# Optimization experiments

Measured on AMD Instinct MI355X. Metric: run time of the kernel, lower is better.

Reference implementation:

```python
import jax, jax.numpy as jnp
import numpy as np

DEPTH = 6; HEADS = 6; DIM = 384; HD = DIM // HEADS
WS = 14; WINDOW_BLOCKS = (0, 1, 3, 4)
IMG = 512; PATCH = 16; GRID = IMG // PATCH        # 32x32 token grid
PRE_GRID = 14                                      # 224 // 16 pretrain grid
SCALE = HD ** -0.5


def layer_norm(x, w, b, eps=1e-5):
    u = x.mean(-1, keepdims=True)
    s = ((x - u) ** 2).mean(-1, keepdims=True)
    return (x - u) / jnp.sqrt(s + eps) * w + b


def get_rel_pos(size, rel_pos):
    # q_size == k_size here; relative coords in [0, 2*size-2]
    coords = jnp.arange(size)[:, None] - jnp.arange(size)[None, :] + (size - 1)
    return rel_pos[coords]  # (size, size, HD)


def attention(x, qkv_w, qkv_b, proj_w, proj_b, rel_h, rel_w):
    B, H, W, C = x.shape
    N = H * W
    qkv = (x.reshape(B, N, C) @ qkv_w.T + qkv_b).reshape(B, N, 3, HEADS, HD)
    qkv = jnp.moveaxis(qkv, 2, 0).transpose(0, 1, 3, 2, 4)  # (3,B,h,N,d)
    q, k, v = qkv[0], qkv[1], qkv[2]
    attn = jnp.einsum('bhqd,bhkd->bhqk', q * SCALE, k)
    # decomposed relative position bias (ViTDet add_decomposed_rel_pos)
    Rh = get_rel_pos(H, rel_h)  # (H,H,d)
    Rw = get_rel_pos(W, rel_w)  # (W,W,d)
    rq = q.reshape(B, HEADS, H, W, HD)
    bias_h = jnp.einsum('bnhwc,hkc->bnhwk', rq, Rh)  # (B,h,H,W,H)
    bias_w = jnp.einsum('bnhwc,wkc->bnhwk', rq, Rw)  # (B,h,H,W,W)
    attn = (attn.reshape(B, HEADS, H, W, H, W)
            + bias_h[..., :, None] + bias_w[..., None, :]).reshape(B, HEADS, N, N)
    attn = jax.nn.softmax(attn, axis=-1)
    out = jnp.einsum('bhqk,bhkd->bhqd', attn, v)
    out = out.transpose(0, 2, 1, 3).reshape(B, H, W, C)
    return out @ proj_w.T + proj_b


def window_partition(x, ws):
    B, H, W, C = x.shape
    pad_h = (ws - H % ws) % ws
    pad_w = (ws - W % ws) % ws
    x = jnp.pad(x, ((0, 0), (0, pad_h), (0, pad_w), (0, 0)))
    Hp, Wp = H + pad_h, W + pad_w
    x = x.reshape(B, Hp // ws, ws, Wp // ws, ws, C)
    x = x.transpose(0, 1, 3, 2, 4, 5).reshape(-1, ws, ws, C)
    return x, Hp, Wp


def window_unpartition(win, ws, Hp, Wp, H, W):
    B = win.shape[0] // ((Hp // ws) * (Wp // ws))
    x = win.reshape(B, Hp // ws, Wp // ws, ws, ws, -1)
    x = x.transpose(0, 1, 3, 2, 4, 5).reshape(B, Hp, Wp, -1)
    return x[:, :H, :W]


def block(x, p, windowed):
    shortcut = x
    x = layer_norm(x, p['n1w'], p['n1b'])
    if windowed:
        H, W = x.shape[1], x.shape[2]
        x, Hp, Wp = window_partition(x, WS)
    x = attention(x, p['qw'], p['qb'], p['pw'], p['pb'], p['rh'], p['rw'])
    if windowed:
        x = window_unpartition(x, WS, Hp, Wp, H, W)
    x = shortcut + x
    h = layer_norm(x, p['n2w'], p['n2b'])
    h = jax.nn.gelu(h @ p['f1w'].T + p['f1b'], approximate=False)
    return x + h @ p['f2w'].T + p['f2b']


def vit_forward(x, patch_w, patch_b, pos_embed, norm1_w, norm1_b, qkv_w, qkv_b,
                proj_w, proj_b, norm2_w, norm2_b, fc1_w, fc1_b, fc2_w, fc2_b,
                rel_pos_h, rel_pos_w):
    y = jax.lax.conv_general_dilated(
        x, patch_w, (PATCH, PATCH), 'VALID',
        dimension_numbers=('NCHW', 'OIHW', 'NCHW'))
    y = y.transpose(0, 2, 3, 1) + patch_b  # (B, GRID, GRID, DIM)
    # abs pos embed: bicubic resize from pretrain 14x14 grid to 32x32
    pos = pos_embed.reshape(1, PRE_GRID, PRE_GRID, DIM)
    pos = jax.image.resize(pos, (1, GRID, GRID, DIM), 'bicubic')
    y = y + pos
    for i in range(DEPTH):
        windowed = i in WINDOW_BLOCKS
        L = 2 * WS - 1 if windowed else 2 * GRID - 1
        p = dict(n1w=norm1_w[i], n1b=norm1_b[i], qw=qkv_w[i], qb=qkv_b[i],
                 pw=proj_w[i], pb=proj_b[i], rh=rel_pos_h[i, :L], rw=rel_pos_w[i, :L],
                 n2w=norm2_w[i], n2b=norm2_b[i], f1w=fc1_w[i], f1b=fc1_b[i],
                 f2w=fc2_w[i], f2b=fc2_b[i])
        y = block(y, p, windowed)
    return y.transpose(0, 3, 1, 2)  # (B, DIM, GRID, GRID) 'last_feat'


def setup_inputs() -> dict:
    key = jax.random.key(0)
    ks = jax.random.split(key, 10)
    B = 4
    std = 0.02
    f32 = jnp.float32
    return {
        'x': jax.random.normal(ks[0], (B, 3, IMG, IMG), f32),
        'patch_w': jax.random.normal(ks[1], (DIM, 3, PATCH, PATCH), f32) * 0.05,
        'patch_b': jnp.zeros((DIM,), f32),
        'pos_embed': jax.random.normal(ks[2], (1, PRE_GRID * PRE_GRID, DIM), f32) * std,
        'norm1_w': jnp.ones((DEPTH, DIM), f32),
        'norm1_b': jnp.zeros((DEPTH, DIM), f32),
        'qkv_w': jax.random.normal(ks[3], (DEPTH, 3 * DIM, DIM), f32) * std,
        'qkv_b': jnp.zeros((DEPTH, 3 * DIM), f32),
        'proj_w': jax.random.normal(ks[4], (DEPTH, DIM, DIM), f32) * std,
        'proj_b': jnp.zeros((DEPTH, DIM), f32),
        'norm2_w': jnp.ones((DEPTH, DIM), f32),
        'norm2_b': jnp.zeros((DEPTH, DIM), f32),
        'fc1_w': jax.random.normal(ks[5], (DEPTH, 4 * DIM, DIM), f32) * std,
        'fc1_b': jnp.zeros((DEPTH, 4 * DIM), f32),
        'fc2_w': jax.random.normal(ks[6], (DEPTH, DIM, 4 * DIM), f32) * std,
        'fc2_b': jnp.zeros((DEPTH, DIM), f32),
        'rel_pos_h': jax.random.normal(ks[7], (DEPTH, 2 * GRID - 1, HD), f32) * std,
        'rel_pos_w': jax.random.normal(ks[8], (DEPTH, 2 * GRID - 1, HD), f32) * std,
    }


def reference(x, patch_w, patch_b, pos_embed, norm1_w, norm1_b, qkv_w, qkv_b,
              proj_w, proj_b, norm2_w, norm2_b, fc1_w, fc1_b, fc2_w, fc2_b,
              rel_pos_h, rel_pos_w):
    return vit_forward(x, patch_w, patch_b, pos_embed, norm1_w, norm1_b, qkv_w, qkv_b,
                       proj_w, proj_b, norm2_w, norm2_b, fc1_w, fc1_b, fc2_w, fc2_b,
                       rel_pos_h, rel_pos_w)
```

## Files before the change

### kernel.cpp

```cpp
#include <hip/hip_runtime.h>
#include <hip/hip_bf16.h>
#include <math.h>

#define B_SZ 4
#define DIM 384
#define HEADS 6
#define HD 64
#define NTOK 4096
#define WS 14
#define NWIN 36
#define WTOK 196

typedef unsigned short u16;
typedef __bf16 bf16_t;
typedef bf16_t bf16x8 __attribute__((ext_vector_type(8)));
typedef float f32x4 __attribute__((ext_vector_type(4)));

__device__ __forceinline__ float bf2f(unsigned u) { return __uint_as_float(u << 16); }
__device__ __forceinline__ u16 f2bf(float f) {
    unsigned u = __float_as_uint(f);
    unsigned r = (u + 0x7fffu + ((u >> 16) & 1u)) >> 16;
    return (u16)r;
}
__device__ __forceinline__ unsigned pk2bf(float a, float b) {
    __hip_bfloat162 h = __float22bfloat162_rn(make_float2(a, b));
    unsigned r; __builtin_memcpy(&r, &h, 4); return r;
}

__device__ __forceinline__ void ldsload16(const u16* g, u16* l) {
    __builtin_amdgcn_global_load_lds(
        (const __attribute__((address_space(1))) unsigned int*)g,
        (__attribute__((address_space(3))) unsigned int*)l, 16, 0, 0);
}

__device__ __forceinline__ int swz(int r) { return (r ^ (r >> 2)) & 3; }

__device__ inline float cubic_keys(float x) {
    x = fabsf(x);
    if (x <= 1.f) return ((1.5f * x - 2.5f) * x) * x + 1.f;
    if (x < 2.f)  return ((-0.5f * x + 2.5f) * x - 4.f) * x + 2.f;
    return 0.f;
}

__global__ __launch_bounds__(256) void setup_kernel(
        const float* __restrict__ p0, const float* __restrict__ p1,
        const float* __restrict__ p2, const float* __restrict__ p3,
        const float* __restrict__ p4, const float* __restrict__ p5,
        u16* __restrict__ wb, const float* __restrict__ pe,
        float* __restrict__ posr, const float* __restrict__ x,
        u16* __restrict__ col) {
    int i = (blockIdx.x * 256 + threadIdx.x) * 4;
    if (i < 10918656) {
        const float* s; int off;
        if      (i <   294912) { s = p0; off = 0; }
        else if (i <  2949120) { s = p1; off = 294912; }
        else if (i <  3833856) { s = p2; off = 2949120; }
        else if (i <  7372800) { s = p3; off = 3833856; }
        else if (i < 10911744) { s = p4; off = 7372800; }
        else                   { s = p5; off = 10911744; }
        float4 v = *(const float4*)(s + (i - off));
        u16 o[4] = { f2bf(v.x), f2bf(v.y), f2bf(v.z), f2bf(v.w) };
        *(uint2*)(wb + i) = *(const uint2*)o;
        return;
    }
    i -= 10918656;
    if (i < 393216) {
        int c = i % 384;
        int g = i / 384;
        int gy = g / 32, gx = g % 32;
        float wy[14], wx[14];
        float sy = (gy + 0.5f) * (14.f / 32.f) - 0.5f;
        float sx = (gx + 0.5f) * (14.f / 32.f) - 0.5f;
        float toty = 0.f, totx = 0.f;
        #pragma unroll
        for (int k = 0; k < 14; ++k) {
            wy[k] = cubic_keys(sy - (float)k); toty += wy[k];
            wx[k] = cubic_keys(sx - (float)k); totx += wx[k];
        }
        float4 acc = {0.f, 0.f, 0.f, 0.f};
        #pragma unroll 1
        for (int iy = 0; iy < 14; ++iy) {
            if (wy[iy] == 0.f) continue;
            float4 row = {0.f, 0.f, 0.f, 0.f};
            for (int ix = 0; ix < 14; ++ix) {
                if (wx[ix] == 0.f) continue;
                float4 pv = *(const float4*)(pe + (iy * 14 + ix) * 384 + c);
                row.x += wx[ix] * pv.x; row.y += wx[ix] * pv.y;
                row.z += wx[ix] * pv.z; row.w += wx[ix] * pv.w;
            }
            acc.x += wy[iy] * row.x; acc.y += wy[iy] * row.y;
            acc.z += wy[iy] * row.z; acc.w += wy[iy] * row.w;
        }
        float inv = 1.f / (toty * totx);
        acc.x *= inv; acc.y *= inv; acc.z *= inv; acc.w *= inv;
        *(float4*)(posr + i) = acc;
        return;
    }
    i -= 393216;
    if (i < 3145728) {
        int kk = i % 768;
        int p  = i / 768;
        int b  = p / 1024;
        int ph = (p % 1024) / 32;
        int pw = p % 32;
        int c = kk / 256;
        int r = kk % 256;
        int ii = r / 16, j = r % 16;
        float4 v = *(const float4*)(x + (size_t)b * 3 * 512 * 512 +
                                    (size_t)c * 512 * 512 +
                                    (size_t)(ph * 16 + ii) * 512 + (pw * 16 + j));
        u16 o[4] = { f2bf(v.x), f2bf(v.y), f2bf(v.z), f2bf(v.w) };
        *(uint2*)(col + i) = *(const uint2*)o;
    }
}

__global__ __launch_bounds__(256) void ln_kernel(const float* __restrict__ y,
        const float* __restrict__ lw, const float* __restrict__ lb,
        u16* __restrict__ lnout)
{
    int tok = blockIdx.x * 4 + (threadIdx.x >> 6);
    int t = threadIdx.x & 63;
    size_t base = (size_t)tok * 384;
    float v[6];
    float s = 0.f;
    #pragma unroll
    for (int i = 0; i < 6; ++i) {
        v[i] = y[base + t + 64 * i]; s += v[i];
    }
    #pragma unroll
    for (int off = 32; off > 0; off >>= 1) s += __shfl_xor(s, off);
    float mean = s * (1.f / 384.f);
    float vs = 0.f;
    #pragma unroll
    for (int i = 0; i < 6; ++i) { float d = v[i] - mean; vs += d * d; }
    #pragma unroll
    for (int off = 32; off > 0; off >>= 1) vs += __shfl_xor(vs, off);
    float inv = rsqrtf(vs * (1.f / 384.f) + 1e-5f);
    u16* orow = lnout + base;
    #pragma unroll
    for (int i = 0; i < 6; ++i) {
        int c = t + 64 * i;
        orow[c] = f2bf((v[i] - mean) * inv * lw[c] + lb[c]);
    }
}

__global__ __launch_bounds__(256) void out_transpose(const float* __restrict__ y,
        float* __restrict__ outT)
{
    __shared__ float T[64][65];
    int c0 = blockIdx.x * 64, m0 = blockIdx.y * 64;
    int t = threadIdx.x;
    int cl = t & 63, wv = t >> 6;
    #pragma unroll
    for (int r = 0; r < 16; ++r) {
        int ml = wv * 16 + r;
        T[ml][cl] = y[(size_t)(m0 + ml) * 384 + c0 + cl];
    }
    __syncthreads();
    int b = m0 >> 10, g0 = m0 & 1023;
    int gl = t & 63;
    #pragma unroll
    for (int r = 0; r < 16; ++r) {
        int ccl = wv * 16 + r;
        outT[((size_t)(b * 384 + c0 + ccl)) * 1024 + g0 + gl] = T[gl][ccl];
    }
}

__global__ __launch_bounds__(256) void mfma_gemm4(
        const u16* __restrict__ A, const u16* __restrict__ Wt,
        const float* __restrict__ bias,
        u16* __restrict__ outb,
        int M, int N, int K, int act)
{
    __shared__ u16 As[2][8192];
    __shared__ u16 Bs[2][4096];
    int t = threadIdx.x;
    int lane = t & 63, wave = t >> 6;
    int wm = (wave >> 1) * 64, wn = (wave & 1) * 32;
    int m0 = blockIdx.y * 128, n0 = blockIdx.x * 64;

    int r0 = t >> 2,        c0 = ((t & 3) ^ swz(t >> 2)) * 8;
    int r1 = 64 + (t >> 2), c1 = ((t & 3) ^ swz(64 + (t >> 2))) * 8;
    const u16* a0 = A + (size_t)(m0 + r0) * K + c0;
    const u16* a1 = A + (size_t)(m0 + r1) * K + c1;
    const u16* b0 = Wt + (size_t)(n0 + r0) * K + c0;

    auto stage = [&](int k0, int buf) {
        ldsload16(a0 + k0,      &As[buf][wave * 512]);
        ldsload16(a1 + k0,      &As[buf][2048 + wave * 512]);
        ldsload16(b0 + k0,      &Bs[buf][wave * 512]);
        ldsload16(a0 + k0 + 32, &As[buf][4096 + wave * 512]);
        ldsload16(a1 + k0 + 32, &As[buf][6144 + wave * 512]);
        ldsload16(b0 + k0 + 32, &Bs[buf][2048 + wave * 512]);
    };

    f32x4 acc[4][2] = {};
    int row_a = wm + (lane & 15);
    int row_b = wn + (lane & 15);
    int lq = lane >> 4;
    int nchunks = K / 64;

    stage(0, 0);
    __syncthreads();

    for (int ci = 0; ci < nchunks; ++ci) {
        int p = ci & 1;
        bool pref = (ci + 1 < nchunks);
        if (pref) stage((ci + 1) * 64, 1 - p);
        #pragma unroll
        for (int hf = 0; hf < 2; ++hf) {
            bf16x8 af[4], bfr[2];
            #pragma unroll
            for (int i = 0; i < 4; ++i) {
                int r = row_a + i * 16;
                af[i] = *(const bf16x8*)&As[p][hf * 4096 + r * 32 + ((lq ^ swz(r)) * 8)];
            }
            #pragma unroll
            for (int j = 0; j < 2; ++j) {
                int r = row_b + j * 16;
                bfr[j] = *(const bf16x8*)&Bs[p][hf * 2048 + r * 32 + ((lq ^ swz(r)) * 8)];
            }
            #pragma unroll
            for (int i = 0; i < 4; ++i)
                #pragma unroll
                for (int j = 0; j < 2; ++j)
                    acc[i][j] = __builtin_amdgcn_mfma_f32_16x16x32_bf16(
                        af[i], bfr[j], acc[i][j], 0, 0, 0);
        }
        if (pref) __syncthreads();
    }

    int colq = lane & 15, rowq = (lane >> 4) * 4;
    #pragma unroll
    for (int i = 0; i < 4; ++i) {
        #pragma unroll
        for (int rr = 0; rr < 4; ++rr) {
            int m = m0 + wm + i * 16 + rowq + rr;
            size_t mo = (size_t)m * N;
            #pragma unroll
            for (int j = 0; j < 2; ++j) {
                int n = n0 + wn + j * 16 + colq;
                float v = acc[i][j][rr] + bias[n];
                if (act)  v = 0.5f * v * (1.f + erff(v * 0.70710678118654752f));
                outb[mo + n] = f2bf(v);
            }
        }
    }
}

__global__ __launch_bounds__(256) void mfma_gemm32(
        const u16* __restrict__ A, const u16* __restrict__ Wt,
        const float* __restrict__ bias, const float* __restrict__ posr,
        float* __restrict__ y, int addy, int M, int N, int K)
{
    __shared__ u16 As[2][4096];
    __shared__ u16 Bs[2][2048];
    int t = threadIdx.x;
    int lane = t & 63, wave = t >> 6;
    int wm = (wave >> 1) * 32, wn = (wave & 1) * 16;
    int m0 = blockIdx.y * 64, n0 = blockIdx.x * 32;

    int r0 = t >> 2, c0 = ((t & 3) ^ swz(t >> 2)) * 8;
    const u16* a0 = A + (size_t)(m0 + r0) * K + c0;
    int tb = t & 127;
    int rb = tb >> 2, cb = ((tb & 3) ^ swz(tb >> 2)) * 8;
    const u16* b0 = Wt + (size_t)(n0 + rb) * K + cb;

    auto stage = [&](int k0, int buf) {
        ldsload16(a0 + k0,      &As[buf][wave * 512]);
        ldsload16(a0 + k0 + 32, &As[buf][2048 + wave * 512]);
        if (wave < 2) ldsload16(b0 + k0,      &Bs[buf][wave * 512]);
        else          ldsload16(b0 + k0 + 32, &Bs[buf][1024 + (wave - 2) * 512]);
    };

    f32x4 acc[2] = {};
    int row_a = wm + (lane & 15);
    int row_b = wn + (lane & 15);
    int lq = lane >> 4;
    int nchunks = K / 64;

    stage(0, 0);
    __syncthreads();

    for (int ci = 0; ci < nchunks; ++ci) {
        int p = ci & 1;
        bool pref = (ci + 1 < nchunks);
        if (pref) stage((ci + 1) * 64, 1 - p);
        #pragma unroll
        for (int hf = 0; hf < 2; ++hf) {
            bf16x8 af[2], bf0;
            #pragma unroll
            for (int i = 0; i < 2; ++i) {
                int r = row_a + i * 16;
                af[i] = *(const bf16x8*)&As[p][hf * 2048 + r * 32 + ((lq ^ swz(r)) * 8)];
            }
            {
                int r = row_b;
                bf0 = *(const bf16x8*)&Bs[p][hf * 1024 + r * 32 + ((lq ^ swz(r)) * 8)];
            }
            #pragma unroll
            for (int i = 0; i < 2; ++i)
                acc[i] = __builtin_amdgcn_mfma_f32_16x16x32_bf16(
                    af[i], bf0, acc[i], 0, 0, 0);
        }
        if (pref) __syncthreads();
    }

    int colq = lane & 15, rowq = (lane >> 4) * 4;
    #pragma unroll
    for (int i = 0; i < 2; ++i) {
        #pragma unroll
        for (int rr = 0; rr < 4; ++rr) {
            int m = m0 + wm + i * 16 + rowq + rr;
            size_t mo = (size_t)m * N;
            int n = n0 + wn + colq;
            float v = acc[i][rr] + bias[n];
            if (posr) v += posr[(size_t)(m & 1023) * 384 + n];
            if (addy) v += y[mo + n];
            y[mo + n] = v;
        }
    }
}

template<int N, int W>
__global__ __launch_bounds__(256) void attn_mfma(const u16* __restrict__ qkv,
        const u16* __restrict__ qkb, const float* __restrict__ rh,
        const float* __restrict__ rw, u16* __restrict__ outb,
        float* __restrict__ opart, float* __restrict__ lpart)
{
    constexpr int JS = (W == 32) ? 64 : 32;
    constexpr int L  = (W == 32) ? 63 : 27;
    constexpr int CTR = W - 1;
    constexpr int KSPAN = (W == 32) ? 512 : 224;
    constexpr int NKT = KSPAN / 32;
    __shared__ u16 KV[11776];
    __shared__ u16 bhl[64 * 66];
    __shared__ u16 bwl[64 * 66];
    __shared__ u16 Qt[64 * 66];
    __shared__ unsigned kofs[224];

    u16* Pb = KV + 9216;
    u16* Rt = KV;

    int t = threadIdx.x, lane = t & 63, wave = t >> 6;
    int quad = lane >> 4, l15 = lane & 15;
    int uh = blockIdx.x, qb0 = blockIdx.y * 64;
    int z = (W == 32) ? blockIdx.z : 0;
    int kstart = z * KSPAN;
    int h = uh % HEADS, u = uh / HEADS;
    size_t tbase = (size_t)u * 1024;
    int wb_ = u / 9, wr = u - wb_ * 9;
    int wy = wr / 3, wx = wr - wy * 3;

    auto tok14 = [&](int iy, int ix) -> const u16* {
        int gy = wy * WS + iy, gx = wx * WS + ix;
        if (gy < 32 && gx < 32)
            return qkv + (size_t)(wb_ * 1024 + gy * 32 + gx) * 1152;
        return qkb;
    };
    auto rowptr = [&](int lq2) -> const u16* {
        if constexpr (W == 32) {
            return qkv + (tbase + lq2) * 1152;
        } else {
            int iy = lq2 / WS, ix = lq2 - iy * WS;
            return tok14(iy, ix);
        }
    };

    {
        int q = t & 63, ch0 = (t >> 6) * 16;
        int qc = qb0 + q; if (qc >= N) qc = N - 1;
        const u16* qp = rowptr(qc) + h * 64 + ch0;
        uint4 a = *(const uint4*)qp;
        uint4 b = *(const uint4*)(qp + 8);
        u16 vals[16];
        *(uint4*)vals = a; *(uint4*)(vals + 8) = b;
        #pragma unroll
        for (int c = 0; c < 16; ++c)
            Qt[(ch0 + c) * 66 + q] = ((qb0 + q) < N) ? vals[c] : (u16)0;
    }

    if constexpr (W != 32) {
        if (t < 224) {
            int kh = t / WS;
            kofs[t] = (unsigned)kh | ((unsigned)(t - kh * WS) << 16);
        }
    }

    for (int idx = t; idx < JS * 16; idx += 256) {
        int table = (idx >= JS * 8) ? 1 : 0;
        int id2 = idx & (JS * 8 - 1);
        int j = id2 >> 3, cc0 = (id2 & 7) * 8;
        const float* tab = table ? rw : rh;
        u16 tmp[8];
        if (j < L) {
            const float* src = tab + (size_t)j * 64 + cc0;
            #pragma unroll
            for (int c = 0; c < 8; ++c) tmp[c] = f2bf(src[c]);
        } else {
            #pragma unroll
            for (int c = 0; c < 8; ++c) tmp[c] = 0;
        }
        *(uint4*)&Rt[table * JS * 72 + j * 72 + cc0] = *(uint4*)tmp;
    }
    __syncthreads();

    {
        int tb0 = (W == 32) ? 0 : (wave >> 1);
        int ntb = (W == 32) ? 2 : 1;
        int jt  = (W == 32) ? wave : (wave & 1);
        for (int tt = 0; tt < ntb; ++tt) {
            int table = tb0 + tt;
            const u16* Rtt = Rt + table * JS * 72;
            bf16x8 af0 = *(const bf16x8*)&Rtt[(jt * 16 + l15) * 72 + quad * 8];
            bf16x8 af1 = *(const bf16x8*)&Rtt[(jt * 16 + l15) * 72 + 32 + quad * 8];
            u16* dst = table ? bwl : bhl;
            #pragma unroll
            for (int qt = 0; qt < 4; ++qt) {
                bf16x8 qf0, qf1;
                u16* p0 = (u16*)&qf0; u16* p1 = (u16*)&qf1;
                #pragma unroll
                for (int zz = 0; zz < 8; ++zz) {
                    p0[zz] = Qt[(quad * 8 + zz) * 66 + qt * 16 + l15];
                    p1[zz] = Qt[(32 + quad * 8 + zz) * 66 + qt * 16 + l15];
                }
                f32x4 acc = {};
                acc = __builtin_amdgcn_mfma_f32_16x16x32_bf16(af0, qf0, acc, 0, 0, 0);
                acc = __builtin_amdgcn_mfma_f32_16x16x32_bf16(af1, qf1, acc, 0, 0, 0);
                #pragma unroll
                for (int r = 0; r < 4; ++r)
                    dst[(qt * 16 + l15) * 66 + jt * 16 + quad * 4 + r] = f2bf(acc[r]);
            }
        }
    }
    __syncthreads();

    int skey = (wave * 64 + lane) >> 3;
    int sc8  = ((wave * 64 + lane) & 7) ^ (skey & 7);
    int vkey = t & 31, vch0 = (t >> 5) * 8;
    int siy = 0, six = 0, viy = 0, vix = 0;
    if constexpr (W != 32) {
        int k0 = kstart + skey;
        siy = k0 / WS; six = k0 - siy * WS;
        int k1 = kstart + vkey;
        viy = k1 / WS; vix = k1 - viy * WS;
    }
    auto adv = [](int& iy, int& ix) { ix += 4; iy += 2; if (ix >= WS) { ix -= WS; ++iy; } };

    {
        const u16* kp = (W == 32) ? qkv + (tbase + kstart + skey) * 1152
                                  : tok14(siy, six);
        ldsload16(kp + 384 + h * 64 + sc8 * 8, KV + wave * 512);
        const u16* vp = (W == 32) ? qkv + (tbase + kstart + vkey) * 1152
                                  : tok14(viy, vix);
        uint4 vv = *(const uint4*)(vp + 768 + h * 64 + vch0);
        u16 tmp[8]; *(uint4*)tmp = vv;
        u16* vdst = KV + 4096;
        #pragma unroll
        for (int c = 0; c < 8; ++c) vdst[(vch0 + c) * 40 + vkey] = tmp[c];
        if constexpr (W != 32) { adv(siy, six); adv(viy, vix); }
    }

    bf16x8 qf[2];
    #pragma unroll
    for (int hc = 0; hc < 2; ++hc) {
        u16* qv = (u16*)&qf[hc];
        #pragma unroll
        for (int j = 0; j < 8; ++j)
            qv[j] = Qt[(hc * 32 + quad * 8 + j) * 66 + wave * 16 + l15];
    }
    int qme = wave * 16 + l15;
    bool wactive = (W == 32) ? true : ((qb0 + wave * 16) < N);
    int qq = qb0 + qme; if (qq >= N) qq = N - 1;
    int qh = qq / W, qw = qq - qh * W;
    int qh13 = qh + CTR, qw13 = qw + CTR;
    float bwreg[2][4];
    if constexpr (W == 32) {
        #pragma unroll
        for (int kc2 = 0; kc2 < 2; ++kc2)
            #pragma unroll
            for (int r = 0; r < 4; ++r) {
                int keyl = kc2 * 16 + quad * 4 + r;
                bwreg[kc2][r] = bf2f(bwl[qme * 66 + (qw - keyl + CTR)]);
            }
    }

    f32x4 of[4] = {};
    float lsum = 0.f;
    __syncthreads();

    for (int kt = 0; kt < NKT; ++kt) {
        int kb = kstart + kt * 32;
        int p = kt & 1;
        const u16* ksp = KV + p * 2048;
        const u16* vtp = KV + 4096 + p * 2560;
        bool pref = (kt + 1 < NKT);
        uint4 vpref;
        if (pref) {
            const u16* kp = (W == 32) ? qkv + (tbase + kb + 32 + skey) * 1152
                                      : tok14(siy, six);
            ldsload16(kp + 384 + h * 64 + sc8 * 8, KV + (1 - p) * 2048 + wave * 512);
            const u16* vp = (W == 32) ? qkv + (tbase + kb + 32 + vkey) * 1152
                                      : tok14(viy, vix);
            vpref = *(const uint4*)(vp + 768 + h * 64 + vch0);
            if constexpr (W != 32) { adv(siy, six); adv(viy, vix); }
        }

        if (wactive) {
            f32x4 st[2] = {};
            #pragma unroll
            for (int hc = 0; hc < 2; ++hc) {
                #pragma unroll
                for (int kc2 = 0; kc2 < 2; ++kc2) {
                    int key = kc2 * 16 + l15;
                    int c8 = hc * 4 + quad;
                    int pp = key * 8 + (c8 ^ (key & 7));
                    bf16x8 kf = *(const bf16x8*)&ksp[pp * 8];
                    st[kc2] = __builtin_amdgcn_mfma_f32_16x16x32_bf16(
                        kf, qf[hc], st[kc2], 0, 0, 0);
                }
            }
            float bh_t = 0.f;
            if constexpr (W == 32) bh_t = bf2f(bhl[qme * 66 + (qh - (kb >> 5) + CTR)]);
            #pragma unroll
            for (int kc2 = 0; kc2 < 2; ++kc2) {
                float pv4[4];
                #pragma unroll
                for (int r = 0; r < 4; ++r) {
                    int keyl = kc2 * 16 + quad * 4 + r;
                    float pv;
                    if constexpr (W == 32) {
                        float b = bh_t + bwreg[kc2][r];
                        pv = __expf(fmaf(st[kc2][r], 0.125f, b));
                    } else {
                        unsigned ko = kofs[kb + keyl];
                        float b = bf2f(bhl[qme * 66 + qh13 - (int)(ko & 0xffffu)]) +
                                  bf2f(bwl[qme * 66 + qw13 - (int)(ko >> 16)]);
                        pv = __expf(fmaf(st[kc2][r], 0.125f, b));
                        if (kb + keyl >= N) pv = 0.f;
                    }
                    lsum += pv;
                    pv4[r] = pv;
                }
                uint2 pk;
                pk.x = pk2bf(pv4[0], pv4[1]);
                pk.y = pk2bf(pv4[2], pv4[3]);
                *(uint2*)&Pb[wave * 640 + l15 * 40 + kc2 * 16 + quad * 4] = pk;
            }
            bf16x8 pf = *(const bf16x8*)&Pb[wave * 640 + l15 * 40 + quad * 8];
            #pragma unroll
            for (int ca = 0; ca < 4; ++ca) {
                bf16x8 vf = *(const bf16x8*)&vtp[(ca * 16 + l15) * 40 + quad * 8];
                of[ca] = __builtin_amdgcn_mfma_f32_16x16x32_bf16(
                    vf, pf, of[ca], 0, 0, 0);
            }
        }

        if (pref) {
            u16 tmp[8]; *(uint4*)tmp = vpref;
            u16* vdst = KV + 4096 + (1 - p) * 2560;
            #pragma unroll
            for (int c = 0; c < 8; ++c) vdst[(vch0 + c) * 40 + vkey] = tmp[c];
            __syncthreads();
        }
    }

    lsum += __shfl_xor(lsum, 16);
    lsum += __shfl_xor(lsum, 32);
    int q = qb0 + qme;
    if constexpr (W == 32) {
        size_t ridx = (size_t)z * 24576 + (size_t)uh * 1024 + q;
        float* op = opart + ridx * 64;
        #pragma unroll
        for (int ca = 0; ca < 4; ++ca)
            *(float4*)&op[ca * 16 + quad * 4] = (float4){of[ca][0], of[ca][1],
                                                         of[ca][2], of[ca][3]};
        if (quad == 0) lpart[ridx] = lsum;
    } else {
        float inv = 1.f / lsum;
        if (q < N) {
            int iy = q / WS, ix = q - iy * WS;
            int gy = wy * WS + iy, gx = wx * WS + ix;
            if (gy >= 32 || gx >= 32) return;
            u16* op = outb + (size_t)(wb_ * 1024 + gy * 32 + gx) * 384 + h * 64;
            #pragma unroll
            for (int ca = 0; ca < 4; ++ca) {
                uint2 pk;
                pk.x = pk2bf(of[ca][0] * inv, of[ca][1] * inv);
                pk.y = pk2bf(of[ca][2] * inv, of[ca][3] * inv);
                *(uint2*)&op[ca * 16 + quad * 4] = pk;
            }
        }
    }
}

__global__ __launch_bounds__(256) void attn_merge_kernel(const float* __restrict__ O,
        const float* __restrict__ Lp, u16* __restrict__ attb)
{
    int gi = blockIdx.x * 256 + threadIdx.x;
    int idx = gi >> 4;
    int ch = (gi & 15) * 4;
    float4 o0 = *(const float4*)&O[(size_t)idx * 64 + ch];
    float4 o1 = *(const float4*)&O[((size_t)24576 + idx) * 64 + ch];
    float inv = 1.f / (Lp[idx] + Lp[24576 + idx]);
    int uh = idx >> 10, q = idx & 1023;
    int u = uh / 6, h = uh - u * 6;
    uint2 pk;
    pk.x = pk2bf((o0.x + o1.x) * inv, (o0.y + o1.y) * inv);
    pk.y = pk2bf((o0.z + o1.z) * inv, (o0.w + o1.w) * inv);
    *(uint2*)(attb + ((size_t)(u * 1024 + q)) * 384 + h * 64 + ch) = pk;
}

static inline void launch_gemm(const u16* A, const u16* W, const float* bias,
                               u16* outb, int M, int N, int K, int act,
                               hipStream_t s) {
    dim3 g(N / 64, M / 128, 1);
    mfma_gemm4<<<g, 256, 0, s>>>(A, W, bias, outb, M, N, K, act);
}

static inline void launch_gemm32(const u16* A, const u16* W, const float* bias,
                                 const float* posr, float* y, int addy,
                                 int M, int N, int K, hipStream_t s) {
    dim3 g(N / 32, M / 64, 1);
    mfma_gemm32<<<g, 256, 0, s>>>(A, W, bias, posr, y, addy, M, N, K);
}

extern "C" void kernel_launch(void* const* d_in, const int* in_sizes, int n_in,
                              void* d_out, int out_size, void* d_ws, size_t ws_size,
                              hipStream_t stream) {
    const float* x      = (const float*)d_in[0];
    const float* patchw = (const float*)d_in[1];
    const float* patchb = (const float*)d_in[2];
    const float* pos    = (const float*)d_in[3];
    const float* n1w    = (const float*)d_in[4];
    const float* n1b    = (const float*)d_in[5];
    const float* qkvw   = (const float*)d_in[6];
    const float* qkvb   = (const float*)d_in[7];
    const float* pw     = (const float*)d_in[8];
    const float* pb     = (const float*)d_in[9];
    const float* n2w    = (const float*)d_in[10];
    const float* n2b    = (const float*)d_in[11];
    const float* f1w    = (const float*)d_in[12];
    const float* f1b    = (const float*)d_in[13];
    const float* f2w    = (const float*)d_in[14];
    const float* f2b    = (const float*)d_in[15];
    const float* rph    = (const float*)d_in[16];
    const float* rpw    = (const float*)d_in[17];
    float* out = (float*)d_out;

    float* y   = (float*)d_ws;
    u16* attb  = (u16*)(y + 1572864);
    u16* mlpb  = attb + 1572864;
    u16* lnb   = mlpb + 6291456;
    u16* qkvx  = lnb + 1572864;
    u16* rsrv  = qkvx + 4718592;
    u16* wb    = rsrv + 7864320;
    float* posr = (float*)(wb + 10918656);

    u16* colb  = rsrv;
    float* Opart   = (float*)mlpb;
    float* Lpart   = (float*)lnb;

    u16* wb_patch = wb;
    u16* wb_qkv   = wb + 294912;
    u16* wb_pw    = wb + 2949120;
    u16* wb_f1    = wb + 3833856;
    u16* wb_f2    = wb + 7372800;
    u16* wqb      = wb + 10911744;

    setup_kernel<<<(14457600 / 4 + 255) / 256, 256, 0, stream>>>(
        patchw, qkvw, pw, f1w, f2w, qkvb, wb, pos, posr, x, colb);

    launch_gemm32(colb, wb_patch, patchb, posr, y, 0, NTOK, 384, 768, stream);
    ln_kernel<<<1024, 256, 0, stream>>>(y, n1w, n1b, lnb);

    for (int i = 0; i < 6; ++i) {
        bool windowed = (i == 0 || i == 1 || i == 3 || i == 4);
        const float* rh = rph + (size_t)i * 63 * 64;
        const float* rw = rpw + (size_t)i * 63 * 64;
        launch_gemm(lnb, wb_qkv + (size_t)i * 442368, qkvb + i * 1152,
                    qkvx, NTOK, 1152, 384, 0, stream);
        if (windowed) {
            attn_mfma<WTOK, WS><<<dim3(NWIN * HEADS, 4, 1), 256, 0, stream>>>(
                qkvx, wqb + i * 1152, rh, rw, attb, nullptr, nullptr);
        } else {
            attn_mfma<1024, 32><<<dim3(B_SZ * HEADS, 16, 2), 256, 0, stream>>>(
                qkvx, wqb + i * 1152, rh, rw, nullptr, Opart, Lpart);
            attn_merge_kernel<<<1536, 256, 0, stream>>>(Opart, Lpart, attb);
        }
        launch_gemm32(attb, wb_pw + (size_t)i * 147456, pb + i * 384,
                      nullptr, y, 1, NTOK, 384, 384, stream);
        ln_kernel<<<1024, 256, 0, stream>>>(y, n2w + i * 384, n2b + i * 384, lnb);
        launch_gemm(lnb, wb_f1 + (size_t)i * 589824, f1b + i * 1536,
                    mlpb, NTOK, 1536, 384, 1, stream);
        launch_gemm32(mlpb, wb_f2 + (size_t)i * 589824, f2b + i * 384,
                      nullptr, y, 1, NTOK, 384, 1536, stream);
        if (i < 5)
            ln_kernel<<<1024, 256, 0, stream>>>(y, n1w + (i + 1) * 384,
                                                n1b + (i + 1) * 384, lnb);
        else
            out_transpose<<<dim3(6, 64), 256, 0, stream>>>(y, out);
    }
}
```

Measured before the change: 678.0 us.

## Fuse LayerNorm into full-row GEMM epilogue and retile QKV GEMM

Adds a full-row GEMM kernel in which each block computes 16 rows across all 384 output columns. Its epilogue applies bias, positional embedding and the residual add, then computes LayerNorm in-block and writes the bf16 normalized output. This replaces the separate ln_kernel after the patch-embed GEMM and after the attention projection. The QKV GEMM also moves to a new 64x64-tile kernel to get more blocks than the 128x64 tile. The cost is only 256 blocks with a large B tile in LDS, so each block reloads the whole weight matrix and occupancy may be low.

```diff
diff --git a/kernel.cpp b/kernel.cpp
--- a/kernel.cpp
+++ b/kernel.cpp
@@ -248,9 +248,212 @@
     }
 }
 
+__global__ __launch_bounds__(256) void mfma_gemm64b(
+        const u16* __restrict__ A, const u16* __restrict__ Wt,
+        const float* __restrict__ bias, u16* __restrict__ outb,
+        int M, int N, int K)
+{
+    __shared__ u16 As[2][4096];
+    __shared__ u16 Bs[2][4096];
+    int t = threadIdx.x;
+    int lane = t & 63, wave = t >> 6;
+    int wm = (wave >> 1) * 32, wn = (wave & 1) * 32;
+    int m0 = blockIdx.y * 64, n0 = blockIdx.x * 64;
+
+    int r0 = t >> 2, c0 = ((t & 3) ^ swz(t >> 2)) * 8;
+    const u16* a0 = A + (size_t)(m0 + r0) * K + c0;
+    const u16* b0 = Wt + (size_t)(n0 + r0) * K + c0;
+
+    auto stage = [&](int k0, int buf) {
+        ldsload16(a0 + k0,      &As[buf][wave * 512]);
+        ldsload16(b0 + k0,      &Bs[buf][wave * 512]);
+        ldsload16(a0 + k0 + 32, &As[buf][2048 + wave * 512]);
+        ldsload16(b0 + k0 + 32, &Bs[buf][2048 + wave * 512]);
+    };
+
+    f32x4 acc[2][2] = {};
+    int row_a = wm + (lane & 15);
+    int row_b = wn + (lane & 15);
+    int lq = lane >> 4;
+    int nchunks = K / 64;
+
+    stage(0, 0);
+    __syncthreads();
+
+    for (int ci = 0; ci < nchunks; ++ci) {
+        int p = ci & 1;
+        bool pref = (ci + 1 < nchunks);
+        if (pref) stage((ci + 1) * 64, 1 - p);
+        #pragma unroll
+        for (int hf = 0; hf < 2; ++hf) {
+            bf16x8 af[2], bfr[2];
+            #pragma unroll
+            for (int i = 0; i < 2; ++i) {
+                int r = row_a + i * 16;
+                af[i] = *(const bf16x8*)&As[p][hf * 2048 + r * 32 + ((lq ^ swz(r)) * 8)];
+            }
+            #pragma unroll
+            for (int j = 0; j < 2; ++j) {
+                int r = row_b + j * 16;
+                bfr[j] = *(const bf16x8*)&Bs[p][hf * 2048 + r * 32 + ((lq ^ swz(r)) * 8)];
+            }
+            #pragma unroll
+            for (int i = 0; i < 2; ++i)
+                #pragma unroll
+                for (int j = 0; j < 2; ++j)
+                    acc[i][j] = __builtin_amdgcn_mfma_f32_16x16x32_bf16(
+                        af[i], bfr[j], acc[i][j], 0, 0, 0);
+        }
+        if (pref) __syncthreads();
+    }
+
+    int colq = lane & 15, rowq = (lane >> 4) * 4;
+    #pragma unroll
+    for (int i = 0; i < 2; ++i) {
+        #pragma unroll
+        for (int rr = 0; rr < 4; ++rr) {
+            int m = m0 + wm + i * 16 + rowq + rr;
+            size_t mo = (size_t)m * N;
+            #pragma unroll
+            for (int j = 0; j < 2; ++j) {
+                int n = n0 + wn + j * 16 + colq;
+                outb[mo + n] = f2bf(acc[i][j][rr] + bias[n]);
+            }
+        }
+    }
+}
+
+__global__ __launch_bounds__(256) void mfma_gemm_fr(
+        const u16* __restrict__ A, const u16* __restrict__ Wt,
+        const float* __restrict__ bias, const float* __restrict__ posr,
+        float* __restrict__ y, int addy,
+        const float* __restrict__ lw, const float* __restrict__ lb,
+        u16* __restrict__ lnout, int M, int K)
+{
+    __shared__ u16 As[2][1024];
+    __shared__ u16 Bs[2][24576];
+    __shared__ float red[4][16];
+    int t = threadIdx.x;
+    int lane = t & 63, wave = t >> 6;
+    int quad = lane >> 4, l15 = lane & 15;
+    int m0 = blockIdx.x * 16;
+
+    int arow = lane >> 2;
+    int acol8 = (lane & 3) ^ swz(arow);
+    const u16* asrc = A + (size_t)(m0 + arow) * K + acol8 * 8 + (wave == 1 ? 32 : 0);
+
+    const u16* bsrc[6];
+    #pragma unroll
+    for (int j = 0; j < 6; ++j) {
+        int row = j * 64 + (t >> 2);
+        int col8 = (t & 3) ^ swz(row);
+        bsrc[j] = Wt + (size_t)row * K + col8 * 8;
+    }
+
+    auto stage = [&](int k0, int buf) {
+        #pragma unroll
+        for (int j = 0; j < 6; ++j) {
+            ldsload16(bsrc[j] + k0,      &Bs[buf][(j * 64 + wave * 16) * 32]);
+            ldsload16(bsrc[j] + k0 + 32, &Bs[buf][12288 + (j * 64 + wave * 16) * 32]);
+        }
+        if (wave == 0) ldsload16(asrc + k0, &As[buf][0]);
+        if (wave == 1) ldsload16(asrc + k0, &As[buf][512]);
+    };
+
+    f32x4 acc[6] = {};
+    int nchunks = K / 64;
+
+    stage(0, 0);
+    __syncthreads();
+
+    for (int ci = 0; ci < nchunks; ++ci) {
+        int p = ci & 1;
+        bool pref = (ci + 1 < nchunks);
+        if (pref) stage((ci + 1) * 64, 1 - p);
+        #pragma unroll
+        for (int hf = 0; hf < 2; ++hf) {
+            bf16x8 af = *(const bf16x8*)&As[p][hf * 512 + l15 * 32 +
+                                               ((quad ^ swz(l15)) * 8)];
+            #pragma unroll
+            for (int ct = 0; ct < 6; ++ct) {
+                int rb = wave * 96 + ct * 16 + l15;
+                bf16x8 bfr = *(const bf16x8*)&Bs[p][hf * 12288 + rb * 32 +
+                                                    ((quad ^ swz(rb)) * 8)];
+                acc[ct] = __builtin_amdgcn_mfma_f32_16x16x32_bf16(
+                    af, bfr, acc[ct], 0, 0, 0);
+            }
+        }
+        if (pref) __syncthreads();
+    }
+
+    int colq = l15, rowq = quad * 4;
+    float v[6][4];
+    float s[4] = {0.f, 0.f, 0.f, 0.f};
+    #pragma unroll
+    for (int ct = 0; ct < 6; ++ct) {
+        int n = wave * 96 + ct * 16 + colq;
+        float bn = bias[n];
+        #pragma unroll
+        for (int rr = 0; rr < 4; ++rr) {
+            int m = m0 + rowq + rr;
+            float val = acc[ct][rr] + bn;
+            if (posr) val += posr[(size_t)(m & 1023) * 384 + n];
+            if (addy) val += y[(size_t)m * 384 + n];
+            v[ct][rr] = val;
+            s[rr] += val;
+            y[(size_t)m * 384 + n] = val;
+        }
+    }
+    #pragma unroll
+    for (int off = 1; off < 16; off <<= 1)
+        #pragma unroll
+        for (int rr = 0; rr < 4; ++rr) s[rr] += __shfl_xor(s[rr], off);
+    if (l15 == 0) {
+        #pragma unroll
+        for (int rr = 0; rr < 4; ++rr) red[wave][rowq + rr] = s[rr];
+    }
+    __syncthreads();
+    float mean[4];
+    #pragma unroll
+    for (int rr = 0; rr < 4; ++rr) {
+        float tot = red[0][rowq + rr] + red[1][rowq + rr] +
+                    red[2][rowq + rr] + red[3][rowq + rr];
+        mean[rr] = tot * (1.f / 384.f);
+    }
+    float q2[4] = {0.f, 0.f, 0.f, 0.f};
+    #pragma unroll
+    for (int ct = 0; ct < 6; ++ct)
+        #pragma unroll
+        for (int rr = 0; rr < 4; ++rr) {
+            float d = v[ct][rr] - mean[rr]; q2[rr] += d * d;
+        }
+    #pragma unroll
+    for (int off = 1; off < 16; off <<= 1)
+        #pragma unroll
+        for (int rr = 0; rr < 4; ++rr) q2[rr] += __shfl_xor(q2[rr], off);
+    __syncthreads();
+    if (l15 == 0) {
+        #pragma unroll
+        for (int rr = 0; rr < 4; ++rr) red[wave][rowq + rr] = q2[rr];
+    }
+    __syncthreads();
+    #pragma unroll
+    for (int rr = 0; rr < 4; ++rr) {
+        float tot = red[0][rowq + rr] + red[1][rowq + rr] +
+                    red[2][rowq + rr] + red[3][rowq + rr];
+        float rstd = rsqrtf(tot * (1.f / 384.f) + 1e-5f);
+        #pragma unroll
+        for (int ct = 0; ct < 6; ++ct) {
+            int n = wave * 96 + ct * 16 + colq;
+            lnout[(size_t)(m0 + rowq + rr) * 384 + n] =
+                f2bf((v[ct][rr] - mean[rr]) * rstd * lw[n] + lb[n]);
+        }
+    }
+}
+
 __global__ __launch_bounds__(256) void mfma_gemm32(
         const u16* __restrict__ A, const u16* __restrict__ Wt,
-        const float* __restrict__ bias, const float* __restrict__ posr,
+        const float* __restrict__ bias,
         float* __restrict__ y, int addy, int M, int N, int K)
 {
     __shared__ u16 As[2][4096];
@@ -315,7 +518,6 @@
             size_t mo = (size_t)m * N;
             int n = n0 + wn + colq;
             float v = acc[i][rr] + bias[n];
-            if (posr) v += posr[(size_t)(m & 1023) * 384 + n];
             if (addy) v += y[mo + n];
             y[mo + n] = v;
         }
@@ -618,11 +820,25 @@
     mfma_gemm4<<<g, 256, 0, s>>>(A, W, bias, outb, M, N, K, act);
 }
 
+static inline void launch_gemm64b(const u16* A, const u16* W, const float* bias,
+                                  u16* outb, int M, int N, int K, hipStream_t s) {
+    dim3 g(N / 64, M / 64, 1);
+    mfma_gemm64b<<<g, 256, 0, s>>>(A, W, bias, outb, M, N, K);
+}
+
+static inline void launch_gemm_fr(const u16* A, const u16* W, const float* bias,
+                                  const float* posr, float* y, int addy,
+                                  const float* lw, const float* lb, u16* lnout,
+                                  int M, int K, hipStream_t s) {
+    mfma_gemm_fr<<<M / 16, 256, 0, s>>>(A, W, bias, posr, y, addy, lw, lb,
+                                        lnout, M, K);
+}
+
 static inline void launch_gemm32(const u16* A, const u16* W, const float* bias,
-                                 const float* posr, float* y, int addy,
-                                 int M, int N, int K, hipStream_t s) {
+                                 float* y, int addy, int M, int N, int K,
+                                 hipStream_t s) {
     dim3 g(N / 32, M / 64, 1);
-    mfma_gemm32<<<g, 256, 0, s>>>(A, W, bias, posr, y, addy, M, N, K);
+    mfma_gemm32<<<g, 256, 0, s>>>(A, W, bias, y, addy, M, N, K);
 }
 
 extern "C" void kernel_launch(void* const* d_in, const int* in_sizes, int n_in,
@@ -671,15 +887,15 @@
     setup_kernel<<<(14457600 / 4 + 255) / 256, 256, 0, stream>>>(
         patchw, qkvw, pw, f1w, f2w, qkvb, wb, pos, posr, x, colb);
 
-    launch_gemm32(colb, wb_patch, patchb, posr, y, 0, NTOK, 384, 768, stream);
-    ln_kernel<<<1024, 256, 0, stream>>>(y, n1w, n1b, lnb);
+    launch_gemm_fr(colb, wb_patch, patchb, posr, y, 0, n1w, n1b, lnb,
+                   NTOK, 768, stream);
 
     for (int i = 0; i < 6; ++i) {
         bool windowed = (i == 0 || i == 1 || i == 3 || i == 4);
         const float* rh = rph + (size_t)i * 63 * 64;
         const float* rw = rpw + (size_t)i * 63 * 64;
-        launch_gemm(lnb, wb_qkv + (size_t)i * 442368, qkvb + i * 1152,
-                    qkvx, NTOK, 1152, 384, 0, stream);
+        launch_gemm64b(lnb, wb_qkv + (size_t)i * 442368, qkvb + i * 1152,
+                       qkvx, NTOK, 1152, 384, stream);
         if (windowed) {
             attn_mfma<WTOK, WS><<<dim3(NWIN * HEADS, 4, 1), 256, 0, stream>>>(
                 qkvx, wqb + i * 1152, rh, rw, attb, nullptr, nullptr);
@@ -688,13 +904,13 @@
                 qkvx, wqb + i * 1152, rh, rw, nullptr, Opart, Lpart);
             attn_merge_kernel<<<1536, 256, 0, stream>>>(Opart, Lpart, attb);
         }
-        launch_gemm32(attb, wb_pw + (size_t)i * 147456, pb + i * 384,
-                      nullptr, y, 1, NTOK, 384, 384, stream);
-        ln_kernel<<<1024, 256, 0, stream>>>(y, n2w + i * 384, n2b + i * 384, lnb);
+        launch_gemm_fr(attb, wb_pw + (size_t)i * 147456, pb + i * 384,
+                       nullptr, y, 1, n2w + i * 384, n2b + i * 384, lnb,
+                       NTOK, 384, stream);
         launch_gemm(lnb, wb_f1 + (size_t)i * 589824, f1b + i * 1536,
                     mlpb, NTOK, 1536, 384, 1, stream);
         launch_gemm32(mlpb, wb_f2 + (size_t)i * 589824, f2b + i * 384,
-                      nullptr, y, 1, NTOK, 384, 1536, stream);
+                      y, 1, NTOK, 384, 1536, stream);
         if (i < 5)
             ln_kernel<<<1024, 256, 0, stream>>>(y, n1w + (i + 1) * 384,
                                                 n1b + (i + 1) * 384, lnb);
```

Result: slower. 710.7 us (+4.8%).
